# Optimization experiments

Hardware: AMD Instinct MI355X
Metric: run time of the kernel (lower is better)

## Reference

```python
import jax, jax.numpy as jnp
import numpy as np

S = 1024      # seq_len
H = 768       # hidden_size
L = 50        # num_labels
E = 65536     # num_edges
SW = 10       # span_width


def setup_inputs() -> dict:
    key = jax.random.key(0)
    ks = jax.random.split(key, 10)
    hidden_states = jax.random.normal(ks[0], (1, S, H), jnp.float32)
    src = jax.random.randint(ks[1], (E,), 0, S)
    tgt = jax.random.randint(ks[2], (E,), 0, S)
    lbl = jax.random.randint(ks[3], (E,), 0, L)
    edges = jnp.stack([src, tgt, lbl], axis=-1)[None].astype(jnp.int32)  # [1,E,3]
    gcn_W = (jax.random.normal(ks[4], (L, H, H)) * 0.02).astype(jnp.float32)
    gcn_b = jnp.zeros((L, H), jnp.float32)
    attn_w = (jax.random.normal(ks[5], (H,)) * 0.02).astype(jnp.float32)
    attn_b = jnp.zeros((), jnp.float32)
    D = 3 * H
    ms_W1 = (jax.random.normal(ks[6], (D, D)) * 0.02).astype(jnp.float32)
    ms_b1 = jnp.zeros((D,), jnp.float32)
    ms_W2 = (jax.random.normal(ks[7], (D,)) * 0.02).astype(jnp.float32)
    ms_b2 = jnp.zeros((), jnp.float32)
    ant_W = (jax.random.normal(ks[8], (2 * D,)) * 0.02).astype(jnp.float32)
    ant_b = jnp.zeros((), jnp.float32)
    # candidate spans exactly as generate_candidate_spans with span_width=SW
    starts, ends = [], []
    for i in range(S):
        for j in range(i + 1, min(i + SW, S)):
            starts.append(i)
            ends.append(j)
    span_starts = jnp.asarray(np.array(starts, dtype=np.int32))
    span_ends = jnp.asarray(np.array(ends, dtype=np.int32))
    topk = int(S * 0.4)  # seq_lens*0.4 with all-ones attention mask
    return {
        'hidden_states': hidden_states, 'edges': edges,
        'gcn_W': gcn_W, 'gcn_b': gcn_b,
        'attn_w': attn_w, 'attn_b': attn_b,
        'ms_W1': ms_W1, 'ms_b1': ms_b1, 'ms_W2': ms_W2, 'ms_b2': ms_b2,
        'ant_W': ant_W, 'ant_b': ant_b,
        'span_starts': span_starts, 'span_ends': span_ends, 'topk': topk,
    }


def reference(hidden_states, edges, gcn_W, gcn_b, attn_w, attn_b,
              ms_W1, ms_b1, ms_W2, ms_b2, ant_W, ant_b,
              span_starts, span_ends, topk):
    B, Sq, Hd = hidden_states.shape  # B == 1
    nl = gcn_W.shape[0]
    x = hidden_states[0]  # [S,H]

    # ---- GCNLayer: per-label linear + scatter-add + degree norm + relu ----
    src = edges[0, :, 0]
    tgt = edges[0, :, 1]
    lbl = edges[0, :, 2]
    # aggregate source embeddings by (target,label): equivalent to applying
    # W_l per edge then index_add, since the transform is linear per label.
    seg = tgt * nl + lbl                               # [E]
    src_emb = x[src]                                   # [E,H]  gather
    agg = jax.ops.segment_sum(src_emb, seg, num_segments=Sq * nl)
    agg = agg.reshape(Sq, nl, Hd)                      # [S,L,H]
    cnt = jax.ops.segment_sum(jnp.ones_like(seg, jnp.float32), seg,
                              num_segments=Sq * nl).reshape(Sq, nl)
    out = jnp.einsum('slh,lhd->sd', agg, gcn_W) + cnt @ gcn_b  # [S,H]
    degree = jnp.clip(cnt.sum(axis=1), 1.0)[:, None]
    gcn_out = jax.nn.relu(out / degree)

    # combine_strategy == 'add'
    emb = x + gcn_out                                  # [S,H]

    # ---- SpanRepresentation: attention pooling over each span ----
    offs = jnp.arange(SW)                              # span length <= SW
    pos = span_starts[:, None] + offs                  # [N,SW]
    valid = pos <= span_ends[:, None]
    pos_c = jnp.minimum(pos, Sq - 1)
    win = emb[pos_c]                                   # [N,SW,H] gather
    scores = win @ attn_w + attn_b                     # [N,SW]
    scores = jnp.where(valid, scores, -1e9)
    aw = jax.nn.softmax(scores, axis=1)
    attn_out = jnp.einsum('nw,nwh->nh', aw, win)       # [N,H]
    span_vec = jnp.concatenate([emb[span_starts], emb[span_ends], attn_out],
                               axis=-1)                # [N,3H]

    # ---- MentionScorer ----
    hdn = jax.nn.relu(span_vec @ ms_W1 + ms_b1)
    mention_scores = hdn @ ms_W2 + ms_b2               # [N]

    # ---- prune_spans: top-k ----
    topk_scores, topk_idx = jax.lax.top_k(mention_scores, topk)
    pruned = span_vec[topk_idx]                        # [k,3H]

    # ---- antecedent scores: linear over concat pair == sum of two matvecs ----
    D = span_vec.shape[-1]
    s_i = pruned @ ant_W[:D]                           # [k]
    s_j = pruned @ ant_W[D:]                           # [k]
    ant_scores = s_i[:, None] + s_j[None, :] + ant_b   # [k,k]
    # triu mask (antecedent must strictly precede the mention)
    k = pruned.shape[0]
    triu = jnp.triu(jnp.ones((k, k), bool), k=0)
    ant_scores = jnp.where(triu, -1e4, ant_scores)
    dummy = jnp.zeros((k, 1), ant_scores.dtype)
    ant_scores_with_dummy = jnp.concatenate([dummy, ant_scores], axis=1)  # [k,k+1]
    return ant_scores_with_dummy
```

## Files before the change

### kernel.cpp

```cpp
#include <hip/hip_runtime.h>
#include <stdint.h>

typedef __attribute__((ext_vector_type(4))) float f32x4;
typedef __attribute__((ext_vector_type(4))) int i32x4;
typedef __attribute__((ext_vector_type(8))) int i32x8;

#define S_TOK 1024
#define H_DIM 768
#define NLBL  50
#define NEDGE 65536
#define NSEG  (S_TOK * NLBL)
#define NSPAN 9171
#define MPAD  9216
#define DDIM  2304
#define KTOP  409

__device__ __forceinline__ float bf16u_to_f32(unsigned short h) {
  return __uint_as_float(((unsigned)h) << 16);
}
__device__ __forceinline__ unsigned short pack_fp8x2(float a, float b) {
  return (unsigned short)(__builtin_amdgcn_cvt_pk_fp8_f32(a, b, 0, false) & 0xffff);
}
__device__ __forceinline__ unsigned pack_fp8x4(float a, float b, float c, float d) {
  int v = __builtin_amdgcn_cvt_pk_fp8_f32(a, b, 0, false);
  v = __builtin_amdgcn_cvt_pk_fp8_f32(c, d, v, true);
  return (unsigned)v;
}
__device__ __forceinline__ unsigned char pack_fp8x1(float a) {
  return (unsigned char)(__builtin_amdgcn_cvt_pk_fp8_f32(a, a, 0, false) & 0xff);
}

__device__ __forceinline__ void gl_lds16(const void* g, void* l) {
  __builtin_amdgcn_global_load_lds((const __attribute__((address_space(1))) void*)g,
                                   (__attribute__((address_space(3))) void*)l, 16, 0, 0);
}

__global__ __launch_bounds__(256) void convert_fp8(
    const float* __restrict__ in, unsigned* __restrict__ out, int nquads) {
  int i = blockIdx.x * 256 + threadIdx.x;
  if (i >= nquads) return;
  float4 v = ((const float4*)in)[i];
  out[i] = pack_fp8x4(v.x, v.y, v.z, v.w);
}

__global__ __launch_bounds__(256) void transpose_fp8_b(
    const float* __restrict__ in, unsigned char* __restrict__ out, int R, int C) {
  __shared__ float tile[32][33];
  size_t boff = (size_t)blockIdx.z * R * C;
  int tx = threadIdx.x & 31, ty = threadIdx.x >> 5;
  int c0 = blockIdx.x * 32, r0 = blockIdx.y * 32;
#pragma unroll
  for (int i = 0; i < 4; i++)
    tile[ty + 8 * i][tx] = in[boff + (size_t)(r0 + ty + 8 * i) * C + c0 + tx];
  __syncthreads();
#pragma unroll
  for (int i = 0; i < 4; i++)
    out[boff + (size_t)(c0 + ty + 8 * i) * R + r0 + tx] = pack_fp8x1(tile[tx][ty + 8 * i]);
}

__global__ void edge_count2(const int* __restrict__ edges, int* __restrict__ seg_count,
                            int* __restrict__ tgt_count) {
  int e = blockIdx.x * 256 + threadIdx.x;
  if (e >= NEDGE) return;
  int tgt = edges[e * 3 + 1], lbl = edges[e * 3 + 2];
  atomicAdd(&seg_count[tgt * NLBL + lbl], 1);
  atomicAdd(&tgt_count[tgt], 1);
}

__global__ __launch_bounds__(1024) void scan_t(
    const int* __restrict__ cnt, int* __restrict__ offs) {
  __shared__ int part[1024];
  int t = threadIdx.x;
  int c = cnt[t];
  part[t] = c;
  __syncthreads();
  for (int o = 1; o < 1024; o <<= 1) {
    int v = part[t];
    int u = (t >= o) ? part[t - o] : 0;
    __syncthreads();
    part[t] = v + u;
    __syncthreads();
  }
  offs[t] = part[t] - c;
  if (t == 1023) offs[1024] = part[t];
}

__global__ void edge_scatter_t(const int* __restrict__ edges, const int* __restrict__ tgt_off,
                               int* __restrict__ cursor, int* __restrict__ sorted_row) {
  int e = blockIdx.x * 256 + threadIdx.x;
  if (e >= NEDGE) return;
  int src = edges[e * 3], tgt = edges[e * 3 + 1], lbl = edges[e * 3 + 2];
  int pos = tgt_off[tgt] + atomicAdd(&cursor[tgt], 1);
  sorted_row[pos] = lbl * S_TOK + src;
}

template <int EPI>
__global__ __launch_bounds__(256) void gemm_fp8(
    const unsigned char* __restrict__ A, const unsigned char* __restrict__ B,
    unsigned char* __restrict__ Y, float* __restrict__ C,
    const float* __restrict__ b1, const float* __restrict__ w2,
    int M, int Nn, int Kb, int mb, size_t strideB, size_t strideY) {
  __shared__ unsigned char As[128 * 128];
  __shared__ unsigned char Bs[128 * 128];
  int im = blockIdx.x % mb, in_ = blockIdx.x / mb;
  int m0 = im * 128, n0 = in_ * 128;
  const unsigned char* Bl = B + (size_t)blockIdx.y * strideB;

  int t = threadIdx.x;
  int wave = t >> 6, lane = t & 63;
  int wr = wave >> 1, wc = wave & 1;
  int quad = lane >> 4, l15 = lane & 15;
  int lrow = lane >> 3;
  int lk = ((lane & 7) ^ lrow) << 4;

  f32x4 acc[4][4];
  f32x4 zero = {0.f, 0.f, 0.f, 0.f};
#pragma unroll
  for (int mi = 0; mi < 4; mi++)
#pragma unroll
    for (int ni = 0; ni < 4; ni++) acc[mi][ni] = zero;

  for (int kt = 0; kt < Kb; kt += 128) {
#pragma unroll
    for (int i = 0; i < 4; i++) {
      int c = i * 4 + wave;
      int r = c * 8 + lrow;
      gl_lds16(A + (size_t)(m0 + r) * Kb + kt + lk, &As[c * 1024]);
      gl_lds16(Bl + (size_t)(n0 + r) * Kb + kt + lk, &Bs[c * 1024]);
    }
    __syncthreads();
    i32x8 af[4], bg[4];
#pragma unroll
    for (int mi = 0; mi < 4; mi++) {
      int r = wr * 64 + mi * 16 + l15;
      int base = r * 128;
      i32x4 lo = *(const i32x4*)&As[base + (((2 * quad) ^ (r & 7)) << 4)];
      i32x4 hi = *(const i32x4*)&As[base + (((2 * quad + 1) ^ (r & 7)) << 4)];
      af[mi] = __builtin_shufflevector(lo, hi, 0, 1, 2, 3, 4, 5, 6, 7);
    }
#pragma unroll
    for (int ni = 0; ni < 4; ni++) {
      int r = wc * 64 + ni * 16 + l15;
      int base = r * 128;
      i32x4 lo = *(const i32x4*)&Bs[base + (((2 * quad) ^ (r & 7)) << 4)];
      i32x4 hi = *(const i32x4*)&Bs[base + (((2 * quad + 1) ^ (r & 7)) << 4)];
      bg[ni] = __builtin_shufflevector(lo, hi, 0, 1, 2, 3, 4, 5, 6, 7);
    }
#pragma unroll
    for (int mi = 0; mi < 4; mi++)
#pragma unroll
      for (int ni = 0; ni < 4; ni++)
        acc[mi][ni] = __builtin_amdgcn_mfma_scale_f32_16x16x128_f8f6f4(
            af[mi], bg[ni], acc[mi][ni], 0, 0, 0, 0x7f7f7f7f, 0, 0x7f7f7f7f);
    __syncthreads();
  }

  if (EPI == 0) {
    unsigned char* Yl = Y + (size_t)blockIdx.y * strideY;
#pragma unroll
    for (int mi = 0; mi < 4; mi++)
#pragma unroll
      for (int ni = 0; ni < 4; ni++)
#pragma unroll
        for (int r = 0; r < 4; r++)
          As[(wr * 64 + mi * 16 + quad * 4 + r) * 128 + wc * 64 + ni * 16 + l15] =
              pack_fp8x1(acc[mi][ni][r]);
    __syncthreads();
#pragma unroll
    for (int i = 0; i < 4; i++) {
      int idx = t + i * 256;
      int row = idx >> 3, off2 = (idx & 7) << 4;
      *(i32x4*)(Yl + (size_t)(m0 + row) * Nn + n0 + off2) = *(const i32x4*)&As[row * 128 + off2];
    }
  } else {
    float b1v[4], w2v[4];
#pragma unroll
    for (int ni = 0; ni < 4; ni++) {
      int gn = n0 + wc * 64 + ni * 16 + l15;
      b1v[ni] = b1[gn];
      w2v[ni] = w2[gn];
    }
#pragma unroll
    for (int mi = 0; mi < 4; mi++) {
      int gm = m0 + wr * 64 + mi * 16 + quad * 4;
      float part[4] = {0.f, 0.f, 0.f, 0.f};
#pragma unroll
      for (int ni = 0; ni < 4; ni++)
#pragma unroll
        for (int r = 0; r < 4; r++)
          part[r] += fmaxf(acc[mi][ni][r] + b1v[ni], 0.f) * w2v[ni];
#pragma unroll
      for (int o = 1; o < 16; o <<= 1)
#pragma unroll
        for (int r = 0; r < 4; r++) part[r] += __shfl_xor(part[r], o, 64);
      if (l15 == 0) {
#pragma unroll
        for (int r = 0; r < 4; r++)
          if (gm + r < M) atomicAdd(&C[gm + r], part[r]);
      }
    }
  }
}

__global__ __launch_bounds__(192) void gather_emb_kernel(
    const float* __restrict__ x, const unsigned char* __restrict__ Y,
    const int* __restrict__ tgt_off, const int* __restrict__ sorted_row,
    const int* __restrict__ seg_count, const float* __restrict__ gcn_b,
    float* __restrict__ emb) {
  __shared__ int ed[512];
  int s = blockIdx.x;
  int t = threadIdx.x;
  int b = tgt_off[s], e = tgt_off[s + 1];
  int n = e - b;
  for (int i = t; i < n && i < 512; i += 192) ed[i] = sorted_row[b + i];
  __syncthreads();
  float a0 = 0.f, a1 = 0.f, a2 = 0.f, a3 = 0.f;
  int p = 0;
  for (; p + 1 < n; p += 2) {
    int i0 = (p < 512) ? ed[p] : sorted_row[b + p];
    int i1 = (p + 1 < 512) ? ed[p + 1] : sorted_row[b + p + 1];
    unsigned w0 = ((const unsigned*)(Y + (size_t)i0 * H_DIM))[t];
    unsigned w1 = ((const unsigned*)(Y + (size_t)i1 * H_DIM))[t];
    a0 += __builtin_amdgcn_cvt_f32_fp8(w0, 0) + __builtin_amdgcn_cvt_f32_fp8(w1, 0);
    a1 += __builtin_amdgcn_cvt_f32_fp8(w0, 1) + __builtin_amdgcn_cvt_f32_fp8(w1, 1);
    a2 += __builtin_amdgcn_cvt_f32_fp8(w0, 2) + __builtin_amdgcn_cvt_f32_fp8(w1, 2);
    a3 += __builtin_amdgcn_cvt_f32_fp8(w0, 3) + __builtin_amdgcn_cvt_f32_fp8(w1, 3);
  }
  if (p < n) {
    int i0 = (p < 512) ? ed[p] : sorted_row[b + p];
    unsigned w0 = ((const unsigned*)(Y + (size_t)i0 * H_DIM))[t];
    a0 += __builtin_amdgcn_cvt_f32_fp8(w0, 0);
    a1 += __builtin_amdgcn_cvt_f32_fp8(w0, 1);
    a2 += __builtin_amdgcn_cvt_f32_fp8(w0, 2);
    a3 += __builtin_amdgcn_cvt_f32_fp8(w0, 3);
  }
  float deg = 0.f, b0 = 0.f, b1 = 0.f, b2 = 0.f, b3 = 0.f;
#pragma unroll 5
  for (int l = 0; l < NLBL; l++) {
    float c = (float)seg_count[s * NLBL + l];
    deg += c;
    float4 g = ((const float4*)(gcn_b + l * H_DIM))[t];
    b0 += c * g.x; b1 += c * g.y; b2 += c * g.z; b3 += c * g.w;
  }
  float dinv = 1.f / fmaxf(deg, 1.f);
  float4 xe = ((const float4*)(x + (size_t)s * H_DIM))[t];
  float4 o;
  o.x = xe.x + fmaxf((a0 + b0) * dinv, 0.f);
  o.y = xe.y + fmaxf((a1 + b1) * dinv, 0.f);
  o.z = xe.z + fmaxf((a2 + b2) * dinv, 0.f);
  o.w = xe.w + fmaxf((a3 + b3) * dinv, 0.f);
  ((float4*)(emb + (size_t)s * H_DIM))[t] = o;
}

__global__ __launch_bounds__(256) void span_kernel(
    const float* __restrict__ emb, const float* __restrict__ attn_w,
    unsigned char* __restrict__ spanv) {
  int i = blockIdx.x;
  int nsp = 1023 - i; if (nsp > 9) nsp = 9;
  if (nsp <= 0) return;
  int nrow = nsp + 1;
  __shared__ float rows[10][768];
  __shared__ float dsh[10];
  int t = threadIdx.x;
  for (int idx = t; idx < nrow * 384; idx += 256) {
    int r = idx / 384, c2 = idx % 384;
    float2 v = ((const float2*)(emb + (size_t)(i + r) * H_DIM))[c2];
    rows[r][c2 * 2] = v.x; rows[r][c2 * 2 + 1] = v.y;
  }
  __syncthreads();
  int wave = t >> 6, lane = t & 63;
  for (int w = wave; w < nrow; w += 4) {
    float p = 0.f;
#pragma unroll
    for (int q = 0; q < 12; q++) p += rows[w][lane + 64 * q] * attn_w[lane + 64 * q];
#pragma unroll
    for (int o = 1; o < 64; o <<= 1) p += __shfl_xor(p, o, 64);
    if (lane == 0) dsh[w] = p;
  }
  __syncthreads();
  float d[10], ex[10];
  float mx = -1e30f;
  for (int w = 0; w < nrow; w++) { d[w] = dsh[w]; mx = fmaxf(mx, d[w]); }
  for (int w = 0; w < nrow; w++) ex[w] = __expf(d[w] - mx);
  bool act = (t < 192);
  float n0 = 0.f, n1 = 0.f, n2 = 0.f, n3 = 0.f;
  unsigned s0w = 0;
  if (act) {
    float ra = rows[0][4 * t], rb = rows[0][4 * t + 1];
    float rc = rows[0][4 * t + 2], rd = rows[0][4 * t + 3];
    s0w = pack_fp8x4(ra, rb, rc, rd);
    n0 = ex[0] * ra; n1 = ex[0] * rb; n2 = ex[0] * rc; n3 = ex[0] * rd;
  }
  float S = ex[0];
  int dd = i - 1014;
  int base = 9 * i - (dd > 0 ? dd * (dd - 1) / 2 : 0);
  for (int k = 1; k <= nsp; k++) {
    S += ex[k];
    if (act) {
      float ra = rows[k][4 * t], rb = rows[k][4 * t + 1];
      float rc = rows[k][4 * t + 2], rd = rows[k][4 * t + 3];
      n0 += ex[k] * ra; n1 += ex[k] * rb; n2 += ex[k] * rc; n3 += ex[k] * rd;
      float inv = 1.f / S;
      unsigned* o32 = (unsigned*)(spanv + (size_t)(base + k - 1) * DDIM);
      o32[t]       = s0w;
      o32[192 + t] = pack_fp8x4(ra, rb, rc, rd);
      o32[384 + t] = pack_fp8x4(n0 * inv, n1 * inv, n2 * inv, n3 * inv);
    }
  }
}

__device__ __forceinline__ unsigned score_key(float s) {
  unsigned b = __float_as_uint(s);
  return (b & 0x80000000u) ? ~b : (b | 0x80000000u);
}

__global__ __launch_bounds__(1024) void topk_kernel(
    const float* __restrict__ scores, int* __restrict__ topk_idx) {
  __shared__ unsigned skeys[NSPAN];
  __shared__ int hist[16 * 256];
  __shared__ int hsum[256];
  __shared__ unsigned sh_prefix;
  __shared__ int sh_remaining, sh_cnt;
  __shared__ unsigned long long keys[512];
  int t = threadIdx.x;
  int wv = t >> 6;
  for (int i = t; i < NSPAN; i += 1024) skeys[i] = score_key(scores[i]);
  unsigned prefix = 0;
  int remaining = KTOP;
  for (int p = 3; p >= 0; p--) {
    for (int b = t; b < 16 * 256; b += 1024) hist[b] = 0;
    __syncthreads();
    for (int i = t; i < NSPAN; i += 1024) {
      unsigned u = skeys[i];
      bool ok = (p == 3) ? true : ((u >> ((p + 1) * 8)) == prefix);
      if (ok) atomicAdd(&hist[wv * 256 + ((u >> (p * 8)) & 0xff)], 1);
    }
    __syncthreads();
    if (t < 256) {
      int s = 0;
#pragma unroll
      for (int w = 0; w < 16; w++) s += hist[w * 256 + t];
      hsum[t] = s;
    }
    __syncthreads();
    for (int o = 1; o < 256; o <<= 1) {
      int v = 0, u = 0;
      if (t < 256) { v = hsum[t]; u = (t + o < 256) ? hsum[t + o] : 0; }
      __syncthreads();
      if (t < 256) hsum[t] = v + u;
      __syncthreads();
    }
    if (t < 256) {
      int Sb = hsum[t];
      int Sb1 = (t < 255) ? hsum[t + 1] : 0;
      if (Sb >= remaining && Sb1 < remaining) {
        sh_prefix = (prefix << 8) | (unsigned)t;
        sh_remaining = remaining - Sb1;
      }
    }
    __syncthreads();
    prefix = sh_prefix;
    remaining = sh_remaining;
    __syncthreads();
  }
  unsigned kth = prefix;
  if (t == 0) sh_cnt = 0;
  __syncthreads();
  for (int i = t; i < NSPAN; i += 1024) {
    unsigned u = skeys[i];
    if (u >= kth) {
      int pos = atomicAdd(&sh_cnt, 1);
      if (pos < 512) keys[pos] = (((unsigned long long)(~u)) << 32) | (unsigned)i;
    }
  }
  __syncthreads();
  int cnt = sh_cnt < 512 ? sh_cnt : 512;
  for (int i = t; i < 512; i += 1024)
    if (i >= cnt) keys[i] = ~0ull;
  __syncthreads();
  for (int ksz = 2; ksz <= 512; ksz <<= 1)
    for (int j = ksz >> 1; j > 0; j >>= 1) {
      if (t < 512) {
        int ixj = t ^ j;
        if (ixj > t) {
          unsigned long long a = keys[t], b = keys[ixj];
          bool up = ((t & ksz) == 0);
          if (up ? (a > b) : (a < b)) { keys[t] = b; keys[ixj] = a; }
        }
      }
      __syncthreads();
    }
  for (int i = t; i < KTOP; i += 1024) topk_idx[i] = (int)(keys[i] & 0xffffffffu);
}

__global__ __launch_bounds__(256) void sij_kernel(
    const unsigned char* __restrict__ spanv, const int* __restrict__ topk_idx,
    const float* __restrict__ antW, float* __restrict__ s_i, float* __restrict__ s_j) {
  int r = blockIdx.x;
  int idx = topk_idx[r];
  const unsigned* row32 = (const unsigned*)(spanv + (size_t)idx * DDIM);
  int t = threadIdx.x, lane = t & 63, wave = t >> 6;
  float pi = 0.f, pj = 0.f;
  for (int q = t; q < DDIM / 4; q += 256) {
    unsigned w = row32[q];
    float v0 = __builtin_amdgcn_cvt_f32_fp8(w, 0);
    float v1 = __builtin_amdgcn_cvt_f32_fp8(w, 1);
    float v2 = __builtin_amdgcn_cvt_f32_fp8(w, 2);
    float v3 = __builtin_amdgcn_cvt_f32_fp8(w, 3);
    const float* ai = antW + q * 4;
    const float* aj = antW + DDIM + q * 4;
    pi += v0 * ai[0] + v1 * ai[1] + v2 * ai[2] + v3 * ai[3];
    pj += v0 * aj[0] + v1 * aj[1] + v2 * aj[2] + v3 * aj[3];
  }
  for (int o = 32; o; o >>= 1) {
    pi += __shfl_down(pi, o, 64);
    pj += __shfl_down(pj, o, 64);
  }
  __shared__ float ri[4], rj[4];
  if (lane == 0) { ri[wave] = pi; rj[wave] = pj; }
  __syncthreads();
  if (t == 0) {
    s_i[r] = ri[0] + ri[1] + ri[2] + ri[3];
    s_j[r] = rj[0] + rj[1] + rj[2] + rj[3];
  }
}

__global__ void out_kernel(const float* __restrict__ s_i, const float* __restrict__ s_j,
                           const float* __restrict__ ant_b, float* __restrict__ out) {
  int idx = blockIdx.x * 256 + threadIdx.x;
  if (idx >= KTOP * (KTOP + 1)) return;
  int i = idx / (KTOP + 1), c = idx % (KTOP + 1);
  float v;
  if (c == 0) v = 0.f;
  else {
    int j = c - 1;
    v = (j >= i) ? -10000.f : (s_i[i] + s_j[j] + ant_b[0]);
  }
  out[idx] = v;
}

extern "C" void kernel_launch(void* const* d_in, const int* in_sizes, int n_in,
                              void* d_out, int out_size, void* d_ws, size_t ws_size,
                              hipStream_t stream) {
  const float* x      = (const float*)d_in[0];
  const int*   edges  = (const int*)d_in[1];
  const float* gcn_W  = (const float*)d_in[2];
  const float* gcn_b  = (const float*)d_in[3];
  const float* attn_w = (const float*)d_in[4];
  const float* ms_W1  = (const float*)d_in[6];
  const float* ms_b1  = (const float*)d_in[7];
  const float* ms_W2  = (const float*)d_in[8];
  const float* ant_W  = (const float*)d_in[10];
  const float* ant_b  = (const float*)d_in[11];

  size_t off = 0;
  char* wsb = (char*)d_ws;
  auto alloc = [&](size_t bytes) -> void* {
    void* p = wsb + off;
    off += (bytes + 255) & ~(size_t)255;
    return p;
  };
  unsigned char* Y     = (unsigned char*)alloc((size_t)NLBL * S_TOK * H_DIM);
  unsigned char* WtB   = (unsigned char*)alloc((size_t)NLBL * H_DIM * H_DIM);
  unsigned char* Wt2   = (unsigned char*)alloc((size_t)DDIM * DDIM);
  unsigned char* spanv = (unsigned char*)alloc((size_t)MPAD * DDIM);
  unsigned char* Xb    = (unsigned char*)alloc((size_t)S_TOK * H_DIM);
  int* seg_count  = (int*)alloc(NSEG * 4);
  int* tgt_count  = (int*)alloc(S_TOK * 4);
  int* cursor     = (int*)alloc(S_TOK * 4);
  float* scores   = (float*)alloc(MPAD * 4);
  size_t zero_bytes = (char*)(scores + MPAD) - (char*)seg_count;
  int* tgt_off    = (int*)alloc((S_TOK + 4) * 4);
  int* sorted_row = (int*)alloc(NEDGE * 4);
  float* emb    = (float*)alloc((size_t)S_TOK * H_DIM * 4);
  int* topk_idx = (int*)alloc(512 * 4);
  float* s_i    = (float*)alloc(512 * 4);
  float* s_j    = (float*)alloc(512 * 4);
  (void)ws_size; (void)in_sizes; (void)n_in; (void)out_size;

  hipMemsetAsync(seg_count, 0, zero_bytes, stream);

  dim3 b256(256);
  convert_fp8<<<(S_TOK * H_DIM / 4 + 255) / 256, b256, 0, stream>>>(x, (unsigned*)Xb,
                                                                    S_TOK * H_DIM / 4);
  transpose_fp8_b<<<dim3(H_DIM / 32, H_DIM / 32, NLBL), b256, 0, stream>>>(gcn_W, WtB, H_DIM, H_DIM);
  transpose_fp8_b<<<dim3(DDIM / 32, DDIM / 32, 1), b256, 0, stream>>>(ms_W1, Wt2, DDIM, DDIM);
  edge_count2<<<NEDGE / 256, b256, 0, stream>>>(edges, seg_count, tgt_count);
  scan_t<<<1, 1024, 0, stream>>>(tgt_count, tgt_off);
  edge_scatter_t<<<NEDGE / 256, b256, 0, stream>>>(edges, tgt_off, cursor, sorted_row);
  gemm_fp8<0><<<dim3(48, NLBL), b256, 0, stream>>>(
      Xb, WtB, Y, nullptr, nullptr, nullptr,
      S_TOK, H_DIM, H_DIM, 8, (size_t)H_DIM * H_DIM, (size_t)S_TOK * H_DIM);
  gather_emb_kernel<<<S_TOK, dim3(192), 0, stream>>>(x, Y, tgt_off, sorted_row, seg_count, gcn_b, emb);
  span_kernel<<<S_TOK, b256, 0, stream>>>(emb, attn_w, spanv);
  gemm_fp8<1><<<dim3(72 * 18, 1), b256, 0, stream>>>(
      spanv, Wt2, nullptr, scores, ms_b1, ms_W2,
      NSPAN, DDIM, DDIM, 72, 0, 0);
  topk_kernel<<<1, 1024, 0, stream>>>(scores, topk_idx);
  sij_kernel<<<KTOP, b256, 0, stream>>>(spanv, topk_idx, ant_W, s_i, s_j);
  out_kernel<<<(KTOP * (KTOP + 1) + 255) / 256, b256, 0, stream>>>(s_i, s_j, ant_b, (float*)d_out);
}
```

Measured before the change: 424.8 us.

## Widen fp8 GEMM tiles to two B tiles per block to reuse A

Each GEMM block now loads two B tiles per K step and computes two 128x128 accumulator sets that share one A tile. For the GCN GEMM this means two labels per block; for the mention-scorer GEMM it means a 256-wide N tile. The grid sizes are halved to match. This halves A-tile global loads and LDS A reads per output, at the cost of doubled accumulator registers (128 fp32 per lane), more LDS (48KB), and fewer blocks, which may reduce occupancy.

```diff
diff --git a/kernel.cpp b/kernel.cpp
--- a/kernel.cpp
+++ b/kernel.cpp
@@ -101,10 +101,22 @@
     const float* __restrict__ b1, const float* __restrict__ w2,
     int M, int Nn, int Kb, int mb, size_t strideB, size_t strideY) {
   __shared__ unsigned char As[128 * 128];
-  __shared__ unsigned char Bs[128 * 128];
+  __shared__ unsigned char Bs0[128 * 128];
+  __shared__ unsigned char Bs1[128 * 128];
   int im = blockIdx.x % mb, in_ = blockIdx.x / mb;
-  int m0 = im * 128, n0 = in_ * 128;
-  const unsigned char* Bl = B + (size_t)blockIdx.y * strideB;
+  int m0 = im * 128;
+  int n0 = in_ * (EPI == 1 ? 256 : 128);
+  const unsigned char* B0;
+  const unsigned char* B1;
+  int rb0, rb1;
+  if (EPI == 0) {
+    B0 = B + (size_t)(2 * blockIdx.y) * strideB;
+    B1 = B + (size_t)(2 * blockIdx.y + 1) * strideB;
+    rb0 = n0; rb1 = n0;
+  } else {
+    B0 = B; B1 = B;
+    rb0 = n0; rb1 = n0 + 128;
+  }
 
   int t = threadIdx.x;
   int wave = t >> 6, lane = t & 63;
@@ -113,12 +125,14 @@
   int lrow = lane >> 3;
   int lk = ((lane & 7) ^ lrow) << 4;
 
-  f32x4 acc[4][4];
+  f32x4 acc[2][4][4];
   f32x4 zero = {0.f, 0.f, 0.f, 0.f};
 #pragma unroll
-  for (int mi = 0; mi < 4; mi++)
-#pragma unroll
-    for (int ni = 0; ni < 4; ni++) acc[mi][ni] = zero;
+  for (int j = 0; j < 2; j++)
+#pragma unroll
+    for (int mi = 0; mi < 4; mi++)
+#pragma unroll
+      for (int ni = 0; ni < 4; ni++) acc[j][mi][ni] = zero;
 
   for (int kt = 0; kt < Kb; kt += 128) {
 #pragma unroll
@@ -126,10 +140,11 @@
       int c = i * 4 + wave;
       int r = c * 8 + lrow;
       gl_lds16(A + (size_t)(m0 + r) * Kb + kt + lk, &As[c * 1024]);
-      gl_lds16(Bl + (size_t)(n0 + r) * Kb + kt + lk, &Bs[c * 1024]);
-    }
-    __syncthreads();
-    i32x8 af[4], bg[4];
+      gl_lds16(B0 + (size_t)(rb0 + r) * Kb + kt + lk, &Bs0[c * 1024]);
+      gl_lds16(B1 + (size_t)(rb1 + r) * Kb + kt + lk, &Bs1[c * 1024]);
+    }
+    __syncthreads();
+    i32x8 af[4];
 #pragma unroll
     for (int mi = 0; mi < 4; mi++) {
       int r = wr * 64 + mi * 16 + l15;
@@ -139,56 +154,69 @@
       af[mi] = __builtin_shufflevector(lo, hi, 0, 1, 2, 3, 4, 5, 6, 7);
     }
 #pragma unroll
-    for (int ni = 0; ni < 4; ni++) {
-      int r = wc * 64 + ni * 16 + l15;
-      int base = r * 128;
-      i32x4 lo = *(const i32x4*)&Bs[base + (((2 * quad) ^ (r & 7)) << 4)];
-      i32x4 hi = *(const i32x4*)&Bs[base + (((2 * quad + 1) ^ (r & 7)) << 4)];
-      bg[ni] = __builtin_shufflevector(lo, hi, 0, 1, 2, 3, 4, 5, 6, 7);
-    }
+    for (int j = 0; j < 2; j++) {
+      const unsigned char* Bsj = (j == 0) ? Bs0 : Bs1;
+      i32x8 bg[4];
+#pragma unroll
+      for (int ni = 0; ni < 4; ni++) {
+        int r = wc * 64 + ni * 16 + l15;
+        int base = r * 128;
+        i32x4 lo = *(const i32x4*)&Bsj[base + (((2 * quad) ^ (r & 7)) << 4)];
+        i32x4 hi = *(const i32x4*)&Bsj[base + (((2 * quad + 1) ^ (r & 7)) << 4)];
+        bg[ni] = __builtin_shufflevector(lo, hi, 0, 1, 2, 3, 4, 5, 6, 7);
+      }
+#pragma unroll
+      for (int mi = 0; mi < 4; mi++)
+#pragma unroll
+        for (int ni = 0; ni < 4; ni++)
+          acc[j][mi][ni] = __builtin_amdgcn_mfma_scale_f32_16x16x128_f8f6f4(
+              af[mi], bg[ni], acc[j][mi][ni], 0, 0, 0, 0x7f7f7f7f, 0, 0x7f7f7f7f);
+    }
+    __syncthreads();
+  }
+
+  if (EPI == 0) {
+    unsigned char* Yl0 = Y + (size_t)(2 * blockIdx.y) * strideY;
+    unsigned char* Yl1 = Y + (size_t)(2 * blockIdx.y + 1) * strideY;
 #pragma unroll
     for (int mi = 0; mi < 4; mi++)
 #pragma unroll
       for (int ni = 0; ni < 4; ni++)
-        acc[mi][ni] = __builtin_amdgcn_mfma_scale_f32_16x16x128_f8f6f4(
-            af[mi], bg[ni], acc[mi][ni], 0, 0, 0, 0x7f7f7f7f, 0, 0x7f7f7f7f);
-    __syncthreads();
-  }
-
-  if (EPI == 0) {
-    unsigned char* Yl = Y + (size_t)blockIdx.y * strideY;
-#pragma unroll
-    for (int mi = 0; mi < 4; mi++)
-#pragma unroll
-      for (int ni = 0; ni < 4; ni++)
-#pragma unroll
-        for (int r = 0; r < 4; r++)
-          As[(wr * 64 + mi * 16 + quad * 4 + r) * 128 + wc * 64 + ni * 16 + l15] =
-              pack_fp8x1(acc[mi][ni][r]);
+#pragma unroll
+        for (int r = 0; r < 4; r++) {
+          int off2 = (wr * 64 + mi * 16 + quad * 4 + r) * 128 + wc * 64 + ni * 16 + l15;
+          As[off2]  = pack_fp8x1(acc[0][mi][ni][r]);
+          Bs0[off2] = pack_fp8x1(acc[1][mi][ni][r]);
+        }
     __syncthreads();
 #pragma unroll
     for (int i = 0; i < 4; i++) {
       int idx = t + i * 256;
       int row = idx >> 3, off2 = (idx & 7) << 4;
-      *(i32x4*)(Yl + (size_t)(m0 + row) * Nn + n0 + off2) = *(const i32x4*)&As[row * 128 + off2];
+      *(i32x4*)(Yl0 + (size_t)(m0 + row) * Nn + n0 + off2) = *(const i32x4*)&As[row * 128 + off2];
+      *(i32x4*)(Yl1 + (size_t)(m0 + row) * Nn + n0 + off2) = *(const i32x4*)&Bs0[row * 128 + off2];
     }
   } else {
-    float b1v[4], w2v[4];
-#pragma unroll
-    for (int ni = 0; ni < 4; ni++) {
-      int gn = n0 + wc * 64 + ni * 16 + l15;
-      b1v[ni] = b1[gn];
-      w2v[ni] = w2[gn];
-    }
+    float b1v[2][4], w2v[2][4];
+#pragma unroll
+    for (int j = 0; j < 2; j++)
+#pragma unroll
+      for (int ni = 0; ni < 4; ni++) {
+        int gn = n0 + j * 128 + wc * 64 + ni * 16 + l15;
+        b1v[j][ni] = b1[gn];
+        w2v[j][ni] = w2[gn];
+      }
 #pragma unroll
     for (int mi = 0; mi < 4; mi++) {
       int gm = m0 + wr * 64 + mi * 16 + quad * 4;
       float part[4] = {0.f, 0.f, 0.f, 0.f};
 #pragma unroll
-      for (int ni = 0; ni < 4; ni++)
-#pragma unroll
-        for (int r = 0; r < 4; r++)
-          part[r] += fmaxf(acc[mi][ni][r] + b1v[ni], 0.f) * w2v[ni];
+      for (int j = 0; j < 2; j++)
+#pragma unroll
+        for (int ni = 0; ni < 4; ni++)
+#pragma unroll
+          for (int r = 0; r < 4; r++)
+            part[r] += fmaxf(acc[j][mi][ni][r] + b1v[j][ni], 0.f) * w2v[j][ni];
 #pragma unroll
       for (int o = 1; o < 16; o <<= 1)
 #pragma unroll
@@ -488,12 +516,12 @@
   edge_count2<<<NEDGE / 256, b256, 0, stream>>>(edges, seg_count, tgt_count);
   scan_t<<<1, 1024, 0, stream>>>(tgt_count, tgt_off);
   edge_scatter_t<<<NEDGE / 256, b256, 0, stream>>>(edges, tgt_off, cursor, sorted_row);
-  gemm_fp8<0><<<dim3(48, NLBL), b256, 0, stream>>>(
+  gemm_fp8<0><<<dim3(48, NLBL / 2), b256, 0, stream>>>(
       Xb, WtB, Y, nullptr, nullptr, nullptr,
       S_TOK, H_DIM, H_DIM, 8, (size_t)H_DIM * H_DIM, (size_t)S_TOK * H_DIM);
   gather_emb_kernel<<<S_TOK, dim3(192), 0, stream>>>(x, Y, tgt_off, sorted_row, seg_count, gcn_b, emb);
   span_kernel<<<S_TOK, b256, 0, stream>>>(emb, attn_w, spanv);
-  gemm_fp8<1><<<dim3(72 * 18, 1), b256, 0, stream>>>(
+  gemm_fp8<1><<<dim3(72 * 9, 1), b256, 0, stream>>>(
       spanv, Wt2, nullptr, scores, ms_b1, ms_W2,
       NSPAN, DDIM, DDIM, 72, 0, 0);
   topk_kernel<<<1, 1024, 0, stream>>>(scores, topk_idx);
```

Result: slower. 482.5 us (+13.6%).
